# Kernel optimization log

Hardware: AMD Instinct MI355X
Metric: run time of the kernel (lower is better)

The kernel has to match this reference:

```python
import jax, jax.numpy as jnp
import numpy as np

S, B, E, H = 2048, 32, 512, 512


def _gru_scan(xs, h0, Wih, Whh, bih, bhh):
    """Run a GRUCell recurrence over xs: [T, B, E] with state h0: [B, H].
    PyTorch GRUCell math, gate order (r, z, n)."""
    def step(h, x):
        gx = x @ Wih.T + bih          # [B, 3H]
        gh = h @ Whh.T + bhh          # [B, 3H]
        xr, xz, xn = jnp.split(gx, 3, axis=-1)
        hr, hz, hn = jnp.split(gh, 3, axis=-1)
        r = jax.nn.sigmoid(xr + hr)
        z = jax.nn.sigmoid(xz + hz)
        n = jnp.tanh(xn + r * hn)
        h_new = (1.0 - z) * n + z * h
        return h_new, None
    h_final, _ = jax.lax.scan(step, h0, xs)
    return h_final


def setup_inputs() -> dict:
    key = jax.random.key(0)
    ks = jax.random.split(key, 9)
    k = 1.0 / np.sqrt(H)  # torch GRUCell init bound
    u = lambda kk, shape: jax.random.uniform(kk, shape, jnp.float32, -k, k)
    return {
        "seq_length": S,
        "embedding_seq": jax.random.normal(ks[0], (S, B, E), jnp.float32),
        "Wih_f": u(ks[1], (3 * H, E)),
        "Whh_f": u(ks[2], (3 * H, H)),
        "bih_f": u(ks[3], (3 * H,)),
        "bhh_f": u(ks[4], (3 * H,)),
        "Wih_b": u(ks[5], (3 * H, E)),
        "Whh_b": u(ks[6], (3 * H, H)),
        "bih_b": u(ks[7], (3 * H,)),
        "bhh_b": u(ks[8], (3 * H,)),
    }


def reference(seq_length, embedding_seq, Wih_f, Whh_f, bih_f, bhh_f,
              Wih_b, Whh_b, bih_b, bhh_b):
    xs = embedding_seq[:seq_length]               # [S, B, E]
    h0 = jnp.zeros((xs.shape[1], H), xs.dtype)    # zero initial hidden (init_hiddens)
    hf = _gru_scan(xs, h0, Wih_f, Whh_f, bih_f, bhh_f)          # forward direction
    hb = _gru_scan(xs[::-1], h0, Wih_b, Whh_b, bih_b, bhh_b)    # backward direction
    return jnp.concatenate([hf, hb], axis=1)      # [B, 2H]
```

## Files before the change

kernel.cpp:

```cpp
#include <hip/hip_runtime.h>
#include <stdint.h>

#define S_LEN 2048
#define BATCH 32
#define EDIM  512
#define HDIM  512
#define NSLICE 32
#define SCOLS  16
#define NG     48
#define NTHREADS 512

typedef __attribute__((ext_vector_type(8))) short bf16x8;
typedef __attribute__((ext_vector_type(8))) float f32x8;
typedef __attribute__((ext_vector_type(4))) float f32x4;

__device__ __forceinline__ unsigned short f2bf(float f) {
    union { float f; unsigned int i; } v; v.f = f;
    unsigned int u = v.i;
    return (unsigned short)((u + 0x7fffu + ((u >> 16) & 1u)) >> 16);
}
__device__ __forceinline__ bf16x8 cvt8(f32x8 v) {
    bf16x8 r;
#pragma unroll
    for (int i = 0; i < 8; ++i) r[i] = (short)f2bf(v[i]);
    return r;
}

__global__ void
__attribute__((amdgpu_flat_work_group_size(NTHREADS, NTHREADS)))
__attribute__((amdgpu_waves_per_eu(2, 2)))
gru_persistent(const float* __restrict__ xseq,
               const float* __restrict__ Wih_f,
               const float* __restrict__ Whh_f,
               const float* __restrict__ bih_f,
               const float* __restrict__ bhh_f,
               const float* __restrict__ Wih_b,
               const float* __restrict__ Whh_b,
               const float* __restrict__ bih_b,
               const float* __restrict__ bhh_b,
               float* __restrict__ out,
               int* __restrict__ flags,
               unsigned short* __restrict__ h_buf)
{
    const int wg   = blockIdx.x;
    const int dir  = wg >> 5;
    const int sl   = wg & 31;
    const int tid  = threadIdx.x;
    const int lane = tid & 63;
    const int wv   = tid >> 6;
    const int kh   = wv & 3;
    const int mtw  = wv >> 2;
    const int l15  = lane & 15;
    const int q8   = (lane >> 4) * 8;
    const int rj   = (lane >> 4) * 4;

    const float* Wih = dir ? Wih_b : Wih_f;
    const float* Whh = dir ? Whh_b : Whh_f;
    const float* bih = dir ? bih_b : bih_f;
    const float* bhh = dir ? bhh_b : bhh_f;

    __shared__ float gxl[4][BATCH][NG + 1];
    __shared__ float ghl[4][BATCH][NG + 1];
    __shared__ float hloc[BATCH][SCOLS];
    __shared__ float bih_s[NG], bhh_s[NG];

    bf16x8 wf[3][4], hf[3][4];
    {
#pragma unroll
        for (int ti = 0; ti < 3; ++ti) {
            const int row = ti * HDIM + sl * SCOLS + l15;
#pragma unroll
            for (int kt = 0; kt < 4; ++kt) {
                const int k = kh * 128 + kt * 32 + q8;
                wf[ti][kt] = cvt8(*(const f32x8*)(Wih + (size_t)row * EDIM + k));
                hf[ti][kt] = cvt8(*(const f32x8*)(Whh + (size_t)row * HDIM + k));
            }
        }
    }
    if (tid < NG) {
        const int row = (tid >> 4) * HDIM + sl * SCOLS + (tid & 15);
        bih_s[tid] = bih[row];
        bhh_s[tid] = bhh[row];
    }
    hloc[tid >> 4][tid & 15] = 0.0f;
    __syncthreads();

    const int m_row = mtw * 16 + l15;
    const int kbase = kh * 128;
    int* myflags = flags + dir * NSLICE;

    const int b_pw = tid >> 4;
    const int c_pw = tid & 15;

    bf16x8 xa[4], ha[4];
    {
        const int tx0 = dir ? (S_LEN - 1) : 0;
        const float* xp = xseq + (size_t)tx0 * (BATCH * EDIM)
                          + (size_t)m_row * EDIM + kbase + q8;
#pragma unroll
        for (int kt = 0; kt < 4; ++kt) {
            xa[kt] = cvt8(*(const f32x8*)(xp + kt * 32));
            ha[kt] = bf16x8{};
        }
    }

    for (int t = 0; t < S_LEN; ++t) {
        f32x4 accx[3] = {{0.f,0.f,0.f,0.f},{0.f,0.f,0.f,0.f},{0.f,0.f,0.f,0.f}};
#pragma unroll
        for (int ti = 0; ti < 3; ++ti)
#pragma unroll
            for (int kt = 0; kt < 4; ++kt)
                accx[ti] = __builtin_amdgcn_mfma_f32_16x16x32_bf16(
                               xa[kt], wf[ti][kt], accx[ti], 0, 0, 0);

        if (t > 0) {
            int* fp = myflags + (lane & 31);
            for (;;) {
                int f = __hip_atomic_load(fp, __ATOMIC_RELAXED,
                                          __HIP_MEMORY_SCOPE_AGENT);
                if (__all(f >= t)) break;
            }
            const unsigned short* hp = h_buf
                + ((size_t)((t & 1) * 2 + dir)) * (BATCH * HDIM)
                + (size_t)m_row * HDIM + kbase + q8;
            asm volatile(
                "global_load_dwordx4 %0, %4, off sc1\n\t"
                "global_load_dwordx4 %1, %4, off offset:64  sc1\n\t"
                "global_load_dwordx4 %2, %4, off offset:128 sc1\n\t"
                "global_load_dwordx4 %3, %4, off offset:192 sc1\n\t"
                "s_waitcnt vmcnt(0)"
                : "=v"(ha[0]), "=v"(ha[1]), "=v"(ha[2]), "=v"(ha[3])
                : "v"(hp)
                : "memory");
        }

        f32x4 acch[3] = {{0.f,0.f,0.f,0.f},{0.f,0.f,0.f,0.f},{0.f,0.f,0.f,0.f}};
#pragma unroll
        for (int ti = 0; ti < 3; ++ti)
#pragma unroll
            for (int kt = 0; kt < 4; ++kt)
                acch[ti] = __builtin_amdgcn_mfma_f32_16x16x32_bf16(
                               ha[kt], hf[ti][kt], acch[ti], 0, 0, 0);

#pragma unroll
        for (int ti = 0; ti < 3; ++ti) {
            const int n = ti * 16 + l15;
#pragma unroll
            for (int j = 0; j < 4; ++j) {
                gxl[kh][mtw * 16 + rj + j][n] = accx[ti][j];
                ghl[kh][mtw * 16 + rj + j][n] = acch[ti][j];
            }
        }
        __syncthreads();

        {
            const int b = b_pw, c = c_pw;
            float gxr = gxl[0][b][c]      + gxl[1][b][c]      + gxl[2][b][c]      + gxl[3][b][c];
            float ghr = ghl[0][b][c]      + ghl[1][b][c]      + ghl[2][b][c]      + ghl[3][b][c];
            float gxz = gxl[0][b][16 + c] + gxl[1][b][16 + c] + gxl[2][b][16 + c] + gxl[3][b][16 + c];
            float ghz = ghl[0][b][16 + c] + ghl[1][b][16 + c] + ghl[2][b][16 + c] + ghl[3][b][16 + c];
            float gxn = gxl[0][b][32 + c] + gxl[1][b][32 + c] + gxl[2][b][32 + c] + gxl[3][b][32 + c];
            float ghn = ghl[0][b][32 + c] + ghl[1][b][32 + c] + ghl[2][b][32 + c] + ghl[3][b][32 + c];
            const float xr = gxr + bih_s[c];
            const float hr = ghr + bhh_s[c];
            const float xz = gxz + bih_s[16 + c];
            const float hz = ghz + bhh_s[16 + c];
            const float xn = gxn + bih_s[32 + c];
            const float hn = ghn + bhh_s[32 + c];
            const float r  = 1.f / (1.f + __expf(-(xr + hr)));
            const float z  = 1.f / (1.f + __expf(-(xz + hz)));
            const float pre = xn + r * hn;
            const float n_  = 2.f / (1.f + __expf(-2.f * pre)) - 1.f;
            const float hnew = (1.f - z) * n_ + z * hloc[b][c];
            hloc[b][c] = hnew;
            if (t < S_LEN - 1) {
                const float hother = __shfl_xor(hnew, 1);
                if ((c & 1) == 0) {
                    unsigned int pack = (unsigned int)f2bf(hnew)
                                      | ((unsigned int)f2bf(hother) << 16);
                    unsigned int* dst = (unsigned int*)(h_buf
                        + ((size_t)(((t + 1) & 1) * 2 + dir)) * (BATCH * HDIM)
                        + (size_t)b * HDIM + sl * SCOLS + c);
                    asm volatile("global_store_dword %0, %1, off sc1"
                                 :: "v"(dst), "v"(pack) : "memory");
                }
            } else {
                out[(size_t)b * (2 * HDIM) + dir * HDIM + sl * SCOLS + c] = hnew;
            }
        }
        asm volatile("s_waitcnt vmcnt(0)" ::: "memory");
        __syncthreads();

        if (t < S_LEN - 1) {
            if (tid == 0) {
                __hip_atomic_store(&myflags[sl], t + 1, __ATOMIC_RELAXED,
                                   __HIP_MEMORY_SCOPE_AGENT);
            }
            const int txn = dir ? (S_LEN - 2 - t) : (t + 1);
            const float* xq = xseq + (size_t)txn * (BATCH * EDIM)
                              + (size_t)m_row * EDIM + kbase + q8;
#pragma unroll
            for (int kt = 0; kt < 4; ++kt) {
                f32x8 v = *(const f32x8*)(xq + kt * 32);
                xa[kt] = cvt8(v);
            }
        }
    }
}

extern "C" void kernel_launch(void* const* d_in, const int* in_sizes, int n_in,
                              void* d_out, int out_size, void* d_ws, size_t ws_size,
                              hipStream_t stream) {
    const float* xseq  = (const float*)d_in[1];
    const float* Wih_f = (const float*)d_in[2];
    const float* Whh_f = (const float*)d_in[3];
    const float* bih_f = (const float*)d_in[4];
    const float* bhh_f = (const float*)d_in[5];
    const float* Wih_b = (const float*)d_in[6];
    const float* Whh_b = (const float*)d_in[7];
    const float* bih_b = (const float*)d_in[8];
    const float* bhh_b = (const float*)d_in[9];

    int* flags = (int*)d_ws;
    unsigned short* h_buf = (unsigned short*)((char*)d_ws + 512);
    const size_t init_bytes = 512 + (size_t)2 * 2 * BATCH * HDIM * sizeof(unsigned short);
    hipMemsetAsync(d_ws, 0, init_bytes, stream);

    hipLaunchKernelGGL(gru_persistent, dim3(2 * NSLICE), dim3(NTHREADS), 0, stream,
                       xseq, Wih_f, Whh_f, bih_f, bhh_f,
                       Wih_b, Whh_b, bih_b, bhh_b,
                       (float*)d_out, flags, h_buf);
}
```

Baseline: 10.12 ms.

## Interleave both GRU directions in each workgroup, halving grid to 32 blocks

Each of the 32 workgroups now owns one hidden-column slice for both forward and backward directions and alternates half-steps between them. The K dimension is split over all 8 waves, each covering both batch tiles, instead of 4 K-groups times 2 M-tiles. The idea is to let one direction's flag wait and h exchange overlap with the other direction's compute, and to cut the number of spinning participants. The cost is that each step is serialized per workgroup with twice the barriers, more register pressure from holding both weight sets, and a larger LDS reduction over 8 partials.

Result: slower. 20.46 ms (+102.2%).

```diff
diff --git a/kernel.cpp b/kernel.cpp
--- a/kernel.cpp
+++ b/kernel.cpp
@@ -8,7 +8,9 @@
 #define NSLICE 32
 #define SCOLS  16
 #define NG     48
+#define NKH    8
 #define NTHREADS 512
+#define LPAD   50
 
 typedef __attribute__((ext_vector_type(8))) short bf16x8;
 typedef __attribute__((ext_vector_type(8))) float f32x8;
@@ -24,6 +26,130 @@
 #pragma unroll
     for (int i = 0; i < 8; ++i) r[i] = (short)f2bf(v[i]);
     return r;
+}
+
+template<int DIR>
+__device__ __forceinline__ void half_step(
+    const int t, const int sl, const int tid,
+    const bf16x8 (&wf)[3][2], const bf16x8 (&hf)[3][2],
+    bf16x8 (&xa)[2][2],
+    float (*gxl)[BATCH][LPAD], float (*ghl)[BATCH][LPAD],
+    float (*hloc)[SCOLS],
+    const float* bih_s, const float* bhh_s,
+    const float* __restrict__ xseq,
+    unsigned short* __restrict__ h_buf,
+    int* __restrict__ flags,
+    float* __restrict__ out)
+{
+    const int lane = tid & 63;
+    const int kh   = tid >> 6;
+    const int l15  = lane & 15;
+    const int q8   = (lane >> 4) * 8;
+    const int rj   = (lane >> 4) * 4;
+
+#pragma unroll
+    for (int ti = 0; ti < 3; ++ti)
+#pragma unroll
+        for (int mt = 0; mt < 2; ++mt) {
+            f32x4 a = {0.f, 0.f, 0.f, 0.f};
+#pragma unroll
+            for (int kt = 0; kt < 2; ++kt)
+                a = __builtin_amdgcn_mfma_f32_16x16x32_bf16(
+                        xa[mt][kt], wf[ti][kt], a, 0, 0, 0);
+#pragma unroll
+            for (int j = 0; j < 4; ++j)
+                gxl[kh][mt * 16 + rj + j][ti * 16 + l15] = a[j];
+        }
+
+    bf16x8 ha[2][2] = {};
+    if (t > 0) {
+        int* fp = flags + DIR * NSLICE + kh * 4 + (lane & 3);
+        for (;;) {
+            int f = __hip_atomic_load(fp, __ATOMIC_RELAXED,
+                                      __HIP_MEMORY_SCOPE_AGENT);
+            if (__all(f >= t)) break;
+        }
+        const unsigned short* hp0 = h_buf
+            + ((size_t)((t & 1) * 2 + DIR)) * (BATCH * HDIM)
+            + (size_t)l15 * HDIM + kh * 64 + q8;
+        const unsigned short* hp1 = hp0 + 16 * HDIM;
+        asm volatile(
+            "global_load_dwordx4 %0, %4, off sc1\n\t"
+            "global_load_dwordx4 %1, %4, off offset:64 sc1\n\t"
+            "global_load_dwordx4 %2, %5, off sc1\n\t"
+            "global_load_dwordx4 %3, %5, off offset:64 sc1\n\t"
+            "s_waitcnt vmcnt(0)"
+            : "=v"(ha[0][0]), "=v"(ha[0][1]), "=v"(ha[1][0]), "=v"(ha[1][1])
+            : "v"(hp0), "v"(hp1)
+            : "memory");
+    }
+
+#pragma unroll
+    for (int ti = 0; ti < 3; ++ti)
+#pragma unroll
+        for (int mt = 0; mt < 2; ++mt) {
+            f32x4 a = {0.f, 0.f, 0.f, 0.f};
+#pragma unroll
+            for (int kt = 0; kt < 2; ++kt)
+                a = __builtin_amdgcn_mfma_f32_16x16x32_bf16(
+                        ha[mt][kt], hf[ti][kt], a, 0, 0, 0);
+#pragma unroll
+            for (int j = 0; j < 4; ++j)
+                ghl[kh][mt * 16 + rj + j][ti * 16 + l15] = a[j];
+        }
+
+    __syncthreads();
+
+    {
+        const int b = tid >> 4, c = tid & 15;
+        float sxr = 0.f, shr = 0.f, sxz = 0.f, shz = 0.f, sxn = 0.f, shn = 0.f;
+#pragma unroll
+        for (int k8 = 0; k8 < NKH; ++k8) {
+            sxr += gxl[k8][b][c];        shr += ghl[k8][b][c];
+            sxz += gxl[k8][b][16 + c];   shz += ghl[k8][b][16 + c];
+            sxn += gxl[k8][b][32 + c];   shn += ghl[k8][b][32 + c];
+        }
+        const float xr = sxr + bih_s[c],      hr = shr + bhh_s[c];
+        const float xz = sxz + bih_s[16 + c], hz = shz + bhh_s[16 + c];
+        const float xn = sxn + bih_s[32 + c], hn = shn + bhh_s[32 + c];
+        const float r  = 1.f / (1.f + __expf(-(xr + hr)));
+        const float z  = 1.f / (1.f + __expf(-(xz + hz)));
+        const float pre = xn + r * hn;
+        const float n_  = 2.f / (1.f + __expf(-2.f * pre)) - 1.f;
+        const float hnew = (1.f - z) * n_ + z * hloc[b][c];
+        hloc[b][c] = hnew;
+        if (t < S_LEN - 1) {
+            const float ho = __shfl_xor(hnew, 1);
+            if ((c & 1) == 0) {
+                unsigned int pack = (unsigned int)f2bf(hnew)
+                                  | ((unsigned int)f2bf(ho) << 16);
+                unsigned int* dst = (unsigned int*)(h_buf
+                    + ((size_t)(((t + 1) & 1) * 2 + DIR)) * (BATCH * HDIM)
+                    + (size_t)b * HDIM + sl * SCOLS + c);
+                asm volatile("global_store_dword %0, %1, off sc1"
+                             :: "v"(dst), "v"(pack) : "memory");
+            }
+        } else {
+            out[(size_t)b * (2 * HDIM) + DIR * HDIM + sl * SCOLS + c] = hnew;
+        }
+    }
+    asm volatile("s_waitcnt vmcnt(0)" ::: "memory");
+    __syncthreads();
+
+    if (t < S_LEN - 1) {
+        if (tid == 0) {
+            __hip_atomic_store(&flags[DIR * NSLICE + sl], t + 1,
+                               __ATOMIC_RELAXED, __HIP_MEMORY_SCOPE_AGENT);
+        }
+        const int txn = DIR ? (S_LEN - 2 - t) : (t + 1);
+        const float* xq = xseq + (size_t)txn * (BATCH * EDIM);
+#pragma unroll
+        for (int mt = 0; mt < 2; ++mt)
+#pragma unroll
+            for (int kt = 0; kt < 2; ++kt)
+                xa[mt][kt] = cvt8(*(const f32x8*)(xq
+                    + (size_t)(mt * 16 + l15) * EDIM + kh * 64 + kt * 32 + q8));
+    }
 }
 
 __global__ void
@@ -42,169 +168,56 @@
                int* __restrict__ flags,
                unsigned short* __restrict__ h_buf)
 {
-    const int wg   = blockIdx.x;
-    const int dir  = wg >> 5;
-    const int sl   = wg & 31;
+    const int sl   = blockIdx.x;
     const int tid  = threadIdx.x;
     const int lane = tid & 63;
-    const int wv   = tid >> 6;
-    const int kh   = wv & 3;
-    const int mtw  = wv >> 2;
+    const int kh   = tid >> 6;
     const int l15  = lane & 15;
     const int q8   = (lane >> 4) * 8;
-    const int rj   = (lane >> 4) * 4;
-
-    const float* Wih = dir ? Wih_b : Wih_f;
-    const float* Whh = dir ? Whh_b : Whh_f;
-    const float* bih = dir ? bih_b : bih_f;
-    const float* bhh = dir ? bhh_b : bhh_f;
-
-    __shared__ float gxl[4][BATCH][NG + 1];
-    __shared__ float ghl[4][BATCH][NG + 1];
-    __shared__ float hloc[BATCH][SCOLS];
-    __shared__ float bih_s[NG], bhh_s[NG];
-
-    bf16x8 wf[3][4], hf[3][4];
-    {
-#pragma unroll
-        for (int ti = 0; ti < 3; ++ti) {
-            const int row = ti * HDIM + sl * SCOLS + l15;
-#pragma unroll
-            for (int kt = 0; kt < 4; ++kt) {
-                const int k = kh * 128 + kt * 32 + q8;
-                wf[ti][kt] = cvt8(*(const f32x8*)(Wih + (size_t)row * EDIM + k));
-                hf[ti][kt] = cvt8(*(const f32x8*)(Whh + (size_t)row * HDIM + k));
-            }
+
+    __shared__ float gxl[NKH][BATCH][LPAD];
+    __shared__ float ghl[NKH][BATCH][LPAD];
+    __shared__ float hloc2[2][BATCH][SCOLS];
+    __shared__ float bihS[2][NG], bhhS[2][NG];
+
+    bf16x8 wfF[3][2], hfF[3][2], wfB[3][2], hfB[3][2];
+#pragma unroll
+    for (int ti = 0; ti < 3; ++ti) {
+        const int row = ti * HDIM + sl * SCOLS + l15;
+#pragma unroll
+        for (int kt = 0; kt < 2; ++kt) {
+            const int k = kh * 64 + kt * 32 + q8;
+            wfF[ti][kt] = cvt8(*(const f32x8*)(Wih_f + (size_t)row * EDIM + k));
+            hfF[ti][kt] = cvt8(*(const f32x8*)(Whh_f + (size_t)row * HDIM + k));
+            wfB[ti][kt] = cvt8(*(const f32x8*)(Wih_b + (size_t)row * EDIM + k));
+            hfB[ti][kt] = cvt8(*(const f32x8*)(Whh_b + (size_t)row * HDIM + k));
         }
     }
     if (tid < NG) {
         const int row = (tid >> 4) * HDIM + sl * SCOLS + (tid & 15);
-        bih_s[tid] = bih[row];
-        bhh_s[tid] = bhh[row];
-    }
-    hloc[tid >> 4][tid & 15] = 0.0f;
+        bihS[0][tid] = bih_f[row];  bhhS[0][tid] = bhh_f[row];
+        bihS[1][tid] = bih_b[row];  bhhS[1][tid] = bhh_b[row];
+    }
+    ((float*)hloc2)[tid] = 0.f;
+    ((float*)hloc2)[tid + NTHREADS] = 0.f;
     __syncthreads();
 
-    const int m_row = mtw * 16 + l15;
-    const int kbase = kh * 128;
-    int* myflags = flags + dir * NSLICE;
-
-    const int b_pw = tid >> 4;
-    const int c_pw = tid & 15;
-
-    bf16x8 xa[4], ha[4];
-    {
-        const int tx0 = dir ? (S_LEN - 1) : 0;
-        const float* xp = xseq + (size_t)tx0 * (BATCH * EDIM)
-                          + (size_t)m_row * EDIM + kbase + q8;
-#pragma unroll
-        for (int kt = 0; kt < 4; ++kt) {
-            xa[kt] = cvt8(*(const f32x8*)(xp + kt * 32));
-            ha[kt] = bf16x8{};
-        }
-    }
+    bf16x8 xaF[2][2], xaB[2][2];
+#pragma unroll
+    for (int mt = 0; mt < 2; ++mt)
+#pragma unroll
+        for (int kt = 0; kt < 2; ++kt) {
+            const size_t off = (size_t)(mt * 16 + l15) * EDIM + kh * 64 + kt * 32 + q8;
+            xaF[mt][kt] = cvt8(*(const f32x8*)(xseq + off));
+            xaB[mt][kt] = cvt8(*(const f32x8*)(xseq
+                              + (size_t)(S_LEN - 1) * (BATCH * EDIM) + off));
+        }
 
     for (int t = 0; t < S_LEN; ++t) {
-        f32x4 accx[3] = {{0.f,0.f,0.f,0.f},{0.f,0.f,0.f,0.f},{0.f,0.f,0.f,0.f}};
-#pragma unroll
-        for (int ti = 0; ti < 3; ++ti)
-#pragma unroll
-            for (int kt = 0; kt < 4; ++kt)
-                accx[ti] = __builtin_amdgcn_mfma_f32_16x16x32_bf16(
-                               xa[kt], wf[ti][kt], accx[ti], 0, 0, 0);
-
-        if (t > 0) {
-            int* fp = myflags + (lane & 31);
-            for (;;) {
-                int f = __hip_atomic_load(fp, __ATOMIC_RELAXED,
-                                          __HIP_MEMORY_SCOPE_AGENT);
-                if (__all(f >= t)) break;
-            }
-            const unsigned short* hp = h_buf
-                + ((size_t)((t & 1) * 2 + dir)) * (BATCH * HDIM)
-                + (size_t)m_row * HDIM + kbase + q8;
-            asm volatile(
-                "global_load_dwordx4 %0, %4, off sc1\n\t"
-                "global_load_dwordx4 %1, %4, off offset:64  sc1\n\t"
-                "global_load_dwordx4 %2, %4, off offset:128 sc1\n\t"
-                "global_load_dwordx4 %3, %4, off offset:192 sc1\n\t"
-                "s_waitcnt vmcnt(0)"
-                : "=v"(ha[0]), "=v"(ha[1]), "=v"(ha[2]), "=v"(ha[3])
-                : "v"(hp)
-                : "memory");
-        }
-
-        f32x4 acch[3] = {{0.f,0.f,0.f,0.f},{0.f,0.f,0.f,0.f},{0.f,0.f,0.f,0.f}};
-#pragma unroll
-        for (int ti = 0; ti < 3; ++ti)
-#pragma unroll
-            for (int kt = 0; kt < 4; ++kt)
-                acch[ti] = __builtin_amdgcn_mfma_f32_16x16x32_bf16(
-                               ha[kt], hf[ti][kt], acch[ti], 0, 0, 0);
-
-#pragma unroll
-        for (int ti = 0; ti < 3; ++ti) {
-            const int n = ti * 16 + l15;
-#pragma unroll
-            for (int j = 0; j < 4; ++j) {
-                gxl[kh][mtw * 16 + rj + j][n] = accx[ti][j];
-                ghl[kh][mtw * 16 + rj + j][n] = acch[ti][j];
-            }
-        }
-        __syncthreads();
-
-        {
-            const int b = b_pw, c = c_pw;
-            float gxr = gxl[0][b][c]      + gxl[1][b][c]      + gxl[2][b][c]      + gxl[3][b][c];
-            float ghr = ghl[0][b][c]      + ghl[1][b][c]      + ghl[2][b][c]      + ghl[3][b][c];
-            float gxz = gxl[0][b][16 + c] + gxl[1][b][16 + c] + gxl[2][b][16 + c] + gxl[3][b][16 + c];
-            float ghz = ghl[0][b][16 + c] + ghl[1][b][16 + c] + ghl[2][b][16 + c] + ghl[3][b][16 + c];
-            float gxn = gxl[0][b][32 + c] + gxl[1][b][32 + c] + gxl[2][b][32 + c] + gxl[3][b][32 + c];
-            float ghn = ghl[0][b][32 + c] + ghl[1][b][32 + c] + ghl[2][b][32 + c] + ghl[3][b][32 + c];
-            const float xr = gxr + bih_s[c];
-            const float hr = ghr + bhh_s[c];
-            const float xz = gxz + bih_s[16 + c];
-            const float hz = ghz + bhh_s[16 + c];
-            const float xn = gxn + bih_s[32 + c];
-            const float hn = ghn + bhh_s[32 + c];
-            const float r  = 1.f / (1.f + __expf(-(xr + hr)));
-            const float z  = 1.f / (1.f + __expf(-(xz + hz)));
-            const float pre = xn + r * hn;
-            const float n_  = 2.f / (1.f + __expf(-2.f * pre)) - 1.f;
-            const float hnew = (1.f - z) * n_ + z * hloc[b][c];
-            hloc[b][c] = hnew;
-            if (t < S_LEN - 1) {
-                const float hother = __shfl_xor(hnew, 1);
-                if ((c & 1) == 0) {
-                    unsigned int pack = (unsigned int)f2bf(hnew)
-                                      | ((unsigned int)f2bf(hother) << 16);
-                    unsigned int* dst = (unsigned int*)(h_buf
-                        + ((size_t)(((t + 1) & 1) * 2 + dir)) * (BATCH * HDIM)
-                        + (size_t)b * HDIM + sl * SCOLS + c);
-                    asm volatile("global_store_dword %0, %1, off sc1"
-                                 :: "v"(dst), "v"(pack) : "memory");
-                }
-            } else {
-                out[(size_t)b * (2 * HDIM) + dir * HDIM + sl * SCOLS + c] = hnew;
-            }
-        }
-        asm volatile("s_waitcnt vmcnt(0)" ::: "memory");
-        __syncthreads();
-
-        if (t < S_LEN - 1) {
-            if (tid == 0) {
-                __hip_atomic_store(&myflags[sl], t + 1, __ATOMIC_RELAXED,
-                                   __HIP_MEMORY_SCOPE_AGENT);
-            }
-            const int txn = dir ? (S_LEN - 2 - t) : (t + 1);
-            const float* xq = xseq + (size_t)txn * (BATCH * EDIM)
-                              + (size_t)m_row * EDIM + kbase + q8;
-#pragma unroll
-            for (int kt = 0; kt < 4; ++kt) {
-                f32x8 v = *(const f32x8*)(xq + kt * 32);
-                xa[kt] = cvt8(v);
-            }
-        }
+        half_step<0>(t, sl, tid, wfF, hfF, xaF, gxl, ghl, hloc2[0],
+                     bihS[0], bhhS[0], xseq, h_buf, flags, out);
+        half_step<1>(t, sl, tid, wfB, hfB, xaB, gxl, ghl, hloc2[1],
+                     bihS[1], bhhS[1], xseq, h_buf, flags, out);
     }
 }
 
@@ -223,10 +236,9 @@
 
     int* flags = (int*)d_ws;
     unsigned short* h_buf = (unsigned short*)((char*)d_ws + 512);
-    const size_t init_bytes = 512 + (size_t)2 * 2 * BATCH * HDIM * sizeof(unsigned short);
-    hipMemsetAsync(d_ws, 0, init_bytes, stream);
-
-    hipLaunchKernelGGL(gru_persistent, dim3(2 * NSLICE), dim3(NTHREADS), 0, stream,
+    hipMemsetAsync(d_ws, 0, 512, stream);
+
+    hipLaunchKernelGGL(gru_persistent, dim3(NSLICE), dim3(NTHREADS), 0, stream,
                        xseq, Wih_f, Whh_f, bih_f, bhh_f,
                        Wih_b, Whh_b, bih_b, bhh_b,
                        (float*)d_out, flags, h_buf);
```
